# Performance work log

Hardware: AMD Instinct MI355X
Metric: run time of the kernel (lower is better)

Reference implementation:

```python
import jax, jax.numpy as jnp
import numpy as np

VOCAB = 32000
EMB = 200
HID = 128
B = 64
T = 64


def setup_inputs() -> dict:
    key = jax.random.key(0)
    ks = jax.random.split(key, 10)
    s = 0.05
    return {
        "tokens": jax.random.randint(ks[0], (B, T), 0, VOCAB, dtype=jnp.int32),
        "emb": jax.random.normal(ks[1], (VOCAB, EMB), jnp.float32) * s,
        "W0": jax.random.normal(ks[2], (EMB, 4 * HID), jnp.float32) * s,
        "U0": jax.random.normal(ks[3], (HID, 4 * HID), jnp.float32) * s,
        "b0": jax.random.normal(ks[4], (4 * HID,), jnp.float32) * s,
        "W1": jax.random.normal(ks[5], (HID, 4 * HID), jnp.float32) * s,
        "U1": jax.random.normal(ks[6], (HID, 4 * HID), jnp.float32) * s,
        "b1": jax.random.normal(ks[7], (4 * HID,), jnp.float32) * s,
        "Wout": jax.random.normal(ks[8], (HID, VOCAB), jnp.float32) * s,
        "bout": jax.random.normal(ks[9], (VOCAB,), jnp.float32) * s,
    }


def _lstm_cell(x, h, c, W, U, b):
    # Keras LSTMCell gate order: i, f, g(candidate), o
    z = x @ W + h @ U + b  # [B, 4H]
    i, f, g, o = jnp.split(z, 4, axis=-1)
    c_new = jax.nn.sigmoid(f) * c + jax.nn.sigmoid(i) * jnp.tanh(g)
    h_new = jax.nn.sigmoid(o) * jnp.tanh(c_new)
    return h_new, c_new


def reference(tokens, emb, W0, U0, b0, W1, U1, b1, Wout, bout):
    x = emb[tokens]                      # [B, T, EMB]
    xt = jnp.transpose(x, (1, 0, 2))     # time-major [T, B, EMB]
    zeros = jnp.zeros((tokens.shape[0], HID), x.dtype)
    init = (zeros, zeros, zeros, zeros)  # h0, c0, h1, c1

    def step(carry, xw):
        h0, c0, h1, c1 = carry
        h0, c0 = _lstm_cell(xw, h0, c0, W0, U0, b0)
        h1, c1 = _lstm_cell(h0, h1, c1, W1, U1, b1)
        out = jax.nn.relu(h1 @ Wout + bout)  # [B, VOCAB]
        return (h0, c0, h1, c1), out

    _, outs = jax.lax.scan(step, init, xt)   # [T, B, VOCAB]
    return jnp.transpose(outs, (1, 0, 2))    # [B, T, VOCAB]
```

## Files before the change

kernel.cpp:

```cpp
#include <hip/hip_runtime.h>
#include <stdint.h>
#include <stddef.h>

typedef _Float16 f16;
typedef _Float16 f16x2 __attribute__((ext_vector_type(2)));
typedef _Float16 f16x8 __attribute__((ext_vector_type(8)));
typedef float    f32x4 __attribute__((ext_vector_type(4)));

#define VOCAB 32000
#define EMBD  200
#define HID   128
#define NB    64
#define NT    64
#define G4    (4*HID)

__device__ __forceinline__ float sigf(float x) {
    return __builtin_amdgcn_rcpf(1.f + __expf(-x));
}
__device__ __forceinline__ float tanhf_(float x) {
    return 1.f - 2.f * __builtin_amdgcn_rcpf(1.f + __expf(2.f * x));
}

__global__ __launch_bounds__(256) void k_prep(
    const int* __restrict__ tokens, const float* __restrict__ emb,
    const float* __restrict__ W0, const float* __restrict__ b0,
    const float* __restrict__ U0, const float* __restrict__ W1,
    const float* __restrict__ U1,
    float* __restrict__ z0, uint32_t* __restrict__ wp) {
    const int t = threadIdx.x;
    if (blockIdx.x >= 256) {
        int idx = (blockIdx.x - 256) * 256 + t;
        int m = idx >> 15;
        int rem = idx & 32767;
        int p = rem >> 9, j = rem & 511;
        const float* W = (m == 0) ? U0 : (m == 1) ? W1 : U1;
        f16x2 v;
        v[0] = (f16)W[(2 * p) * G4 + j];
        v[1] = (f16)W[(2 * p + 1) * G4 + j];
        ((f16x2*)wp)[idx] = v;
        return;
    }
    __shared__ __align__(16) float xs[EMBD * 16];
    __shared__ int tok[16];
    const int blk = blockIdx.x;
    if (t < 16) tok[t] = tokens[blk * 16 + t];
    __syncthreads();
    for (int i = t; i < EMBD * 16; i += 256) {
        int r = i / EMBD, k = i - r * EMBD;
        xs[k * 16 + r] = emb[(size_t)tok[r] * EMBD + k];
    }
    __syncthreads();
    const int j = t * 2;
    f32x4 accA[4], accB[4];
#pragma unroll
    for (int grp = 0; grp < 4; ++grp) {
        accA[grp] = f32x4{0.f, 0.f, 0.f, 0.f};
        accB[grp] = f32x4{0.f, 0.f, 0.f, 0.f};
    }
    for (int k = 0; k < EMBD; ++k) {
        float2 w = *(const float2*)(W0 + (size_t)k * G4 + j);
        const f32x4* xv = (const f32x4*)(xs + k * 16);
#pragma unroll
        for (int grp = 0; grp < 4; ++grp) {
            f32x4 x = xv[grp];
            accA[grp] += x * w.x;
            accB[grp] += x * w.y;
        }
    }
    float bx = b0[j], by = b0[j + 1];
#pragma unroll
    for (int grp = 0; grp < 4; ++grp)
#pragma unroll
        for (int r = 0; r < 4; ++r) {
            int row = blk * 16 + grp * 4 + r;
            float2 o; o.x = accA[grp][r] + bx; o.y = accB[grp][r] + by;
            *(float2*)(z0 + (size_t)row * G4 + j) = o;
        }
}

__global__ __launch_bounds__(512, 1) void k_scan(
    const float* __restrict__ z0base, const uint32_t* __restrict__ wp,
    const float* __restrict__ b1, f16* __restrict__ H1,
    const float* __restrict__ Wout, f16* __restrict__ WoutT,
    int role_ofs, int do_wt) {
    __shared__ __align__(16) char smem[17408];
    const int bid = blockIdx.x + role_ofs;
    const int t = threadIdx.x;

    if (bid >= 64) {
        if (!do_wt) return;
        f16* tile = (f16*)smem;
        const int n0 = (bid - 64) * 64;
        for (int i = t; i < 64 * 128; i += 512) {
            int k = i >> 6, n = i & 63;
            tile[n * 136 + k] = (f16)Wout[(size_t)k * VOCAB + n0 + n];
        }
        __syncthreads();
        for (int i = t; i < 1024; i += 512) {
            int n = i >> 4, u = i & 15;
            *(uint4*)(WoutT + (size_t)(n0 + n) * HID + u * 8) =
                *(const uint4*)&tile[n * 136 + u * 8];
        }
        return;
    }

    const int b = bid;
    const int g = t >> 7, q = t & 127;
    float* zA = (float*)smem;
    float* zC = (float*)(smem + 8192);
    f16* h0s = (f16*)(smem + 16384);
    f16* h1s = (f16*)(smem + 16640);

    const f16x8* wp8 = (const f16x8*)wp;
    f16x2 wu0[64], ww1[64], wu1[64];
    const int wbase = (g * 16) * 128 + q;
#pragma unroll
    for (int kk = 0; kk < 16; ++kk) {
        *(f16x8*)&wu0[kk * 4] = wp8[0 * 8192 + wbase + kk * 128];
        *(f16x8*)&ww1[kk * 4] = wp8[1 * 8192 + wbase + kk * 128];
        *(f16x8*)&wu1[kk * 4] = wp8[2 * 8192 + wbase + kk * 128];
    }
    float b1a = 0.f, b1b = 0.f, b1c = 0.f, b1d = 0.f;
    float c0 = 0.f, c1 = 0.f;
    if (t < HID) {
        b1a = b1[t]; b1b = b1[t + 128]; b1c = b1[t + 256]; b1d = b1[t + 384];
        const float* zr = z0base + (size_t)b * NT * G4 + t;
        float zi = zr[0], zg = zr[256], zo = zr[384];
        c0 = sigf(zi) * tanhf_(zg);
        h0s[t] = (f16)(sigf(zo) * tanhf_(c0));
        h1s[t] = (f16)0.f;
    }
    __syncthreads();

    const float* zb = z0base + (size_t)b * NT * G4;
    f16* hout = H1 + (size_t)b * NT * HID;

    for (int s = 0; s < NT; ++s) {
        float za = 0.f, zbv = 0.f, zc = 0.f, zd = 0.f;
        if (t < HID) {
            int nx = (s < 63) ? (s + 1) : 63;
            const float* zr = zb + (size_t)nx * G4 + t;
            za = zr[0]; zbv = zr[128]; zc = zr[256]; zd = zr[384];
        }
        float aA0 = 0.f, aA1 = 0.f, aA2 = 0.f, aA3 = 0.f;
        float aC0 = 0.f, aC1 = 0.f, aC2 = 0.f, aC3 = 0.f;
        {
            f16x2 hh[16];
            const f16x8* hp0 = (const f16x8*)h0s + g * 4;
            *(f16x8*)&hh[0] = hp0[0]; *(f16x8*)&hh[4] = hp0[1];
            *(f16x8*)&hh[8] = hp0[2]; *(f16x8*)&hh[12] = hp0[3];
#pragma unroll
            for (int kk = 0; kk < 16; ++kk) {
                f16x2 h = hh[kk];
                aA0 = __builtin_amdgcn_fdot2(wu0[kk * 4 + 0], h, aA0, false);
                aA1 = __builtin_amdgcn_fdot2(wu0[kk * 4 + 1], h, aA1, false);
                aA2 = __builtin_amdgcn_fdot2(wu0[kk * 4 + 2], h, aA2, false);
                aA3 = __builtin_amdgcn_fdot2(wu0[kk * 4 + 3], h, aA3, false);
                aC0 = __builtin_amdgcn_fdot2(ww1[kk * 4 + 0], h, aC0, false);
                aC1 = __builtin_amdgcn_fdot2(ww1[kk * 4 + 1], h, aC1, false);
                aC2 = __builtin_amdgcn_fdot2(ww1[kk * 4 + 2], h, aC2, false);
                aC3 = __builtin_amdgcn_fdot2(ww1[kk * 4 + 3], h, aC3, false);
            }
            const f16x8* hp1 = (const f16x8*)h1s + g * 4;
            *(f16x8*)&hh[0] = hp1[0]; *(f16x8*)&hh[4] = hp1[1];
            *(f16x8*)&hh[8] = hp1[2]; *(f16x8*)&hh[12] = hp1[3];
#pragma unroll
            for (int kk = 0; kk < 16; ++kk) {
                f16x2 h = hh[kk];
                aC0 = __builtin_amdgcn_fdot2(wu1[kk * 4 + 0], h, aC0, false);
                aC1 = __builtin_amdgcn_fdot2(wu1[kk * 4 + 1], h, aC1, false);
                aC2 = __builtin_amdgcn_fdot2(wu1[kk * 4 + 2], h, aC2, false);
                aC3 = __builtin_amdgcn_fdot2(wu1[kk * 4 + 3], h, aC3, false);
            }
        }
        *(f32x4*)&zA[g * 512 + (q << 2)] = f32x4{aA0, aA1, aA2, aA3};
        *(f32x4*)&zC[g * 512 + (q << 2)] = f32x4{aC0, aC1, aC2, aC3};
        __syncthreads();
        if (t < HID) {
            float z1i = b1a + zC[t]        + zC[512 + t]        + zC[1024 + t]        + zC[1536 + t];
            float z1f = b1b + zC[t + 128]  + zC[512 + t + 128]  + zC[1024 + t + 128]  + zC[1536 + t + 128];
            float z1g = b1c + zC[t + 256]  + zC[512 + t + 256]  + zC[1024 + t + 256]  + zC[1536 + t + 256];
            float z1o = b1d + zC[t + 384]  + zC[512 + t + 384]  + zC[1024 + t + 384]  + zC[1536 + t + 384];
            c1 = sigf(z1f) * c1 + sigf(z1i) * tanhf_(z1g);
            float h1v = sigf(z1o) * tanhf_(c1);
            f16 hf = (f16)h1v;
            h1s[t] = hf;
            hout[s * HID + t] = hf;
            if (s < 63) {
                float z0i = za  + zA[t]       + zA[512 + t]       + zA[1024 + t]       + zA[1536 + t];
                float z0f = zbv + zA[t + 128] + zA[512 + t + 128] + zA[1024 + t + 128] + zA[1536 + t + 128];
                float z0g = zc  + zA[t + 256] + zA[512 + t + 256] + zA[1024 + t + 256] + zA[1536 + t + 256];
                float z0o = zd  + zA[t + 384] + zA[512 + t + 384] + zA[1024 + t + 384] + zA[1536 + t + 384];
                c0 = sigf(z0f) * c0 + sigf(z0i) * tanhf_(z0g);
                h0s[t] = (f16)(sigf(z0o) * tanhf_(c0));
            }
        }
        __syncthreads();
    }
}

__global__ __launch_bounds__(256) void k_gemm2(
    const f16* __restrict__ H1, const f16* __restrict__ WT,
    const float* __restrict__ bout, float* __restrict__ out) {
    __shared__ __align__(16) f16 Asub[2][128 * 128];
    const int t = threadIdx.x;
    const int w = t >> 6, l = t & 63;
    const int lr = l & 15, lk = l >> 4;
    const int n0 = blockIdx.x * 64;

    f16x8 wfrag[4];
#pragma unroll
    for (int ks = 0; ks < 4; ++ks)
        wfrag[ks] = *(const f16x8*)&WT[(size_t)(n0 + w * 16 + lr) * HID + ks * 32 + lk * 8];
    const int ncol = n0 + w * 16 + lk * 4;
    const float4 bv = *(const float4*)&bout[ncol];

    {
        const uint4* Ag = (const uint4*)H1;
#pragma unroll
        for (int i = 0; i < 8; ++i) {
            int Gr = i * 256 + t;
            int row = Gr >> 4, gg = Gr & 15;
            ((uint4*)Asub[0])[(row << 4) | (gg ^ (row & 7))] = Ag[Gr];
        }
    }
    __syncthreads();

    for (int m = 0; m < 32; ++m) {
        const int cur = m & 1;
        if (m < 31) {
            const uint4* Ag = (const uint4*)(H1 + (size_t)(m + 1) * 128 * HID);
#pragma unroll
            for (int i = 0; i < 8; ++i) {
                int Gr = i * 256 + t;
                int row = Gr >> 4, gg = Gr & 15;
                ((uint4*)Asub[cur ^ 1])[(row << 4) | (gg ^ (row & 7))] = Ag[Gr];
            }
        }
        const f16* Ab = Asub[cur];
#pragma unroll
        for (int mt = 0; mt < 8; ++mt) {
            const int row = mt * 16 + lr;
            f32x4 acc = f32x4{0.f, 0.f, 0.f, 0.f};
#pragma unroll
            for (int ks = 0; ks < 4; ++ks) {
                int gg = ks * 4 + lk;
                f16x8 af = *(const f16x8*)&Ab[(row << 7) + ((gg ^ (row & 7)) << 3)];
                acc = __builtin_amdgcn_mfma_f32_16x16x32_f16(wfrag[ks], af, acc, 0, 0, 0);
            }
            float4 o;
            o.x = acc[0] + bv.x; o.y = acc[1] + bv.y;
            o.z = acc[2] + bv.z; o.w = acc[3] + bv.w;
            o.x = o.x > 0.f ? o.x : 0.f;
            o.y = o.y > 0.f ? o.y : 0.f;
            o.z = o.z > 0.f ? o.z : 0.f;
            o.w = o.w > 0.f ? o.w : 0.f;
            *(float4*)&out[(size_t)(m * 128 + row) * VOCAB + ncol] = o;
        }
        __syncthreads();
    }
}

extern "C" void kernel_launch(void* const* d_in, const int* in_sizes, int n_in,
                              void* d_out, int out_size, void* d_ws, size_t ws_size,
                              hipStream_t stream) {
    const int*   tokens = (const int*)d_in[0];
    const float* emb  = (const float*)d_in[1];
    const float* W0   = (const float*)d_in[2];
    const float* U0   = (const float*)d_in[3];
    const float* b0   = (const float*)d_in[4];
    const float* W1   = (const float*)d_in[5];
    const float* U1   = (const float*)d_in[6];
    const float* b1   = (const float*)d_in[7];
    const float* Wout = (const float*)d_in[8];
    const float* bout = (const float*)d_in[9];
    float* out = (float*)d_out;

    char* ws = (char*)d_ws;
    float*    z0base = (float*)ws;
    uint32_t* wp     = (uint32_t*)(ws + 8388608);
    f16*      H1     = (f16*)(ws + 8781824);
    const bool big_ws = ws_size >= (size_t)18026496;
    f16*      WoutT  = big_ws ? (f16*)(ws + 9834496) : (f16*)ws;

    k_prep<<<640, 256, 0, stream>>>(tokens, emb, W0, b0, U0, W1, U1, z0base, wp);
    k_scan<<<564, 512, 0, stream>>>(z0base, wp, b1, H1, Wout, WoutT, 0,
                                    big_ws ? 1 : 0);
    if (!big_ws)
        k_scan<<<500, 512, 0, stream>>>(z0base, wp, b1, H1, Wout, WoutT, 64, 1);
    k_gemm2<<<500, 256, 0, stream>>>(H1, WoutT, bout, out);
}
```

Baseline: 265.6 us.

## Retile output GEMM to 256-column slabs with M-chunk split and nontemporal stores

```diff
diff --git a/kernel.cpp b/kernel.cpp
--- a/kernel.cpp
+++ b/kernel.cpp
@@ -199,24 +199,32 @@
     }
 }
 
-__global__ __launch_bounds__(256) void k_gemm2(
+__global__ __launch_bounds__(256) void k_gemm4(
     const f16* __restrict__ H1, const f16* __restrict__ WT,
     const float* __restrict__ bout, float* __restrict__ out) {
     __shared__ __align__(16) f16 Asub[2][128 * 128];
     const int t = threadIdx.x;
     const int w = t >> 6, l = t & 63;
     const int lr = l & 15, lk = l >> 4;
-    const int n0 = blockIdx.x * 64;
-
-    f16x8 wfrag[4];
-#pragma unroll
-    for (int ks = 0; ks < 4; ++ks)
-        wfrag[ks] = *(const f16x8*)&WT[(size_t)(n0 + w * 16 + lr) * HID + ks * 32 + lk * 8];
-    const int ncol = n0 + w * 16 + lk * 4;
-    const float4 bv = *(const float4*)&bout[ncol];
+    const int slab = blockIdx.x % 125;
+    const int mch  = blockIdx.x / 125;
+    const int n0 = slab * 256;
+    const int mbase0 = mch * 1024;
+
+    f16x8 wfrag[4][4];
+#pragma unroll
+    for (int s = 0; s < 4; ++s)
+#pragma unroll
+        for (int ks = 0; ks < 4; ++ks)
+            wfrag[s][ks] = *(const f16x8*)&WT[
+                (size_t)(n0 + w * 64 + s * 16 + lr) * HID + ks * 32 + lk * 8];
+    f32x4 bv[4];
+#pragma unroll
+    for (int s = 0; s < 4; ++s)
+        bv[s] = *(const f32x4*)&bout[n0 + w * 64 + s * 16 + lk * 4];
 
     {
-        const uint4* Ag = (const uint4*)H1;
+        const uint4* Ag = (const uint4*)(H1 + (size_t)mbase0 * HID);
 #pragma unroll
         for (int i = 0; i < 8; ++i) {
             int Gr = i * 256 + t;
@@ -226,10 +234,10 @@
     }
     __syncthreads();
 
-    for (int m = 0; m < 32; ++m) {
-        const int cur = m & 1;
-        if (m < 31) {
-            const uint4* Ag = (const uint4*)(H1 + (size_t)(m + 1) * 128 * HID);
+    for (int it = 0; it < 8; ++it) {
+        const int cur = it & 1;
+        if (it < 7) {
+            const uint4* Ag = (const uint4*)(H1 + (size_t)(mbase0 + (it + 1) * 128) * HID);
 #pragma unroll
             for (int i = 0; i < 8; ++i) {
                 int Gr = i * 256 + t;
@@ -238,24 +246,29 @@
             }
         }
         const f16* Ab = Asub[cur];
+        const int mb = mbase0 + it * 128;
 #pragma unroll
         for (int mt = 0; mt < 8; ++mt) {
             const int row = mt * 16 + lr;
-            f32x4 acc = f32x4{0.f, 0.f, 0.f, 0.f};
-#pragma unroll
-            for (int ks = 0; ks < 4; ++ks) {
-                int gg = ks * 4 + lk;
-                f16x8 af = *(const f16x8*)&Ab[(row << 7) + ((gg ^ (row & 7)) << 3)];
-                acc = __builtin_amdgcn_mfma_f32_16x16x32_f16(wfrag[ks], af, acc, 0, 0, 0);
-            }
-            float4 o;
-            o.x = acc[0] + bv.x; o.y = acc[1] + bv.y;
-            o.z = acc[2] + bv.z; o.w = acc[3] + bv.w;
-            o.x = o.x > 0.f ? o.x : 0.f;
-            o.y = o.y > 0.f ? o.y : 0.f;
-            o.z = o.z > 0.f ? o.z : 0.f;
-            o.w = o.w > 0.f ? o.w : 0.f;
-            *(float4*)&out[(size_t)(m * 128 + row) * VOCAB + ncol] = o;
+            f16x8 af[4];
+#pragma unroll
+            for (int ks = 0; ks < 4; ++ks)
+                af[ks] = *(const f16x8*)&Ab[(row << 7) + (((ks * 4 + lk) ^ (row & 7)) << 3)];
+            const size_t obase = (size_t)(mb + mt * 16 + lr) * VOCAB + n0 + w * 64 + lk * 4;
+#pragma unroll
+            for (int s = 0; s < 4; ++s) {
+                f32x4 acc = f32x4{0.f, 0.f, 0.f, 0.f};
+                acc = __builtin_amdgcn_mfma_f32_16x16x32_f16(wfrag[s][0], af[0], acc, 0, 0, 0);
+                acc = __builtin_amdgcn_mfma_f32_16x16x32_f16(wfrag[s][1], af[1], acc, 0, 0, 0);
+                acc = __builtin_amdgcn_mfma_f32_16x16x32_f16(wfrag[s][2], af[2], acc, 0, 0, 0);
+                acc = __builtin_amdgcn_mfma_f32_16x16x32_f16(wfrag[s][3], af[3], acc, 0, 0, 0);
+                f32x4 o = acc + bv[s];
+                o[0] = o[0] > 0.f ? o[0] : 0.f;
+                o[1] = o[1] > 0.f ? o[1] : 0.f;
+                o[2] = o[2] > 0.f ? o[2] : 0.f;
+                o[3] = o[3] > 0.f ? o[3] : 0.f;
+                __builtin_nontemporal_store(o, (f32x4*)&out[obase + s * 16]);
+            }
         }
         __syncthreads();
     }
@@ -288,5 +301,5 @@
                                     big_ws ? 1 : 0);
     if (!big_ws)
         k_scan<<<500, 512, 0, stream>>>(z0base, wp, b1, H1, Wout, WoutT, 64, 1);
-    k_gemm2<<<500, 256, 0, stream>>>(H1, WoutT, bout, out);
-}
+    k_gemm4<<<500, 256, 0, stream>>>(H1, WoutT, bout, out);
+}
```

Measured after the change: 293.4 us. 10.4% more time.
